# Kernel optimization log

Measured on AMD Instinct MI355X. Metric: run time of the kernel, lower is better.

Reference implementation:

```python
import jax, jax.numpy as jnp
import numpy as np

B, T, J, D = 64, 800, 50, 200  # batch, context len, query len, 2*hidden

def setup_inputs() -> dict:
    key = jax.random.key(0)
    ks = jax.random.split(key, 8)
    return {
        'h':    jax.random.normal(ks[0], (B, T, D), jnp.float32),
        'u':    jax.random.normal(ks[1], (B, J, D), jnp.float32),
        'w_h':  jax.random.normal(ks[2], (D,), jnp.float32) * 0.05,
        'b_h':  jax.random.normal(ks[3], (1,), jnp.float32) * 0.05,
        'w_u':  jax.random.normal(ks[4], (D,), jnp.float32) * 0.05,
        'b_u':  jax.random.normal(ks[5], (1,), jnp.float32) * 0.05,
        'w_hu': jax.random.normal(ks[6], (D,), jnp.float32) * 0.05,
        'b_hu': jax.random.normal(ks[7], (1,), jnp.float32) * 0.05,
    }

def reference(h, u, w_h, b_h, w_u, b_u, w_hu, b_hu):
    # Similarity: s[b,t,j] = ws_h(h_t) + ws_u(u_j) + ws_hu(h_t * u_j)  (+ summed biases)
    # Computed without materializing the [B,T,J,D] expanded tensors of the original.
    sh = jnp.einsum('btd,d->bt', h, w_h)            # [B,T]
    su = jnp.einsum('bjd,d->bj', u, w_u)            # [B,J]
    shu = jnp.einsum('btd,bjd->btj', h * w_hu, u)   # [B,T,J]
    s = shu + sh[:, :, None] + su[:, None, :] + (b_h + b_u + b_hu)[0]
    # Context-to-query attention
    a = jax.nn.softmax(s, axis=2)                   # [B,T,J]
    c2q = jnp.einsum('btj,bjd->btd', a, u)          # [B,T,D]
    # Query-to-context attention
    b = jax.nn.softmax(jnp.max(s, axis=2), axis=1)  # [B,T]
    q2c = jnp.einsum('bt,btd->bd', b, h)[:, None, :]  # [B,1,D], broadcasts over T
    g = jnp.concatenate([h, c2q, h * c2q, h * q2c], axis=-1)  # [B,T,4D]
    return g
```

## Files before the change

kernel.cpp:

```cpp
#include <hip/hip_runtime.h>
#include <cstdint>
#include <cstddef>

#define B_ 64
#define T_ 800
#define J_ 50
#define D_ 200
#define TILE_T 100
#define NTILE 8
#define TT 5
#define NW 4

__device__ __forceinline__ float dot4(float4 a, float4 b) {
    return fmaf(a.x, b.x, fmaf(a.y, b.y, fmaf(a.z, b.z, a.w * b.w)));
}

__global__ __launch_bounds__(256) void k1_kernel(
    const float* __restrict__ h, const float* __restrict__ u,
    const float* __restrict__ w_h, const float* __restrict__ b_h,
    const float* __restrict__ w_u, const float* __restrict__ b_u,
    const float* __restrict__ w_hu, const float* __restrict__ b_hu,
    float* __restrict__ g, float* __restrict__ smax_ws)
{
    __shared__ __align__(16) float4 u4_s[52][51];
    __shared__ __align__(16) float4 whu4_s[50];
    __shared__ __align__(16) float4 wh4_s[50];
    __shared__ __align__(16) float4 wu4_s[50];
    __shared__ float su_s[52];
    __shared__ __align__(16) float4 hw4_s[NW][TT][50];
    __shared__ __align__(16) float a_s[NW][TT][52];

    const int tid  = threadIdx.x;
    const int b    = blockIdx.x / NTILE;
    const int tile = blockIdx.x % NTILE;

    for (int idx = tid; idx < 52 * 50; idx += 256) {
        int j = idx / 50, k = idx - (idx / 50) * 50;
        float4 v = make_float4(0.f, 0.f, 0.f, 0.f);
        if (j < J_) v = *reinterpret_cast<const float4*>(&u[(b * J_ + j) * D_ + 4 * k]);
        u4_s[j][k] = v;
    }
    if (tid < 50) {
        whu4_s[tid] = *reinterpret_cast<const float4*>(&w_hu[4 * tid]);
        wh4_s[tid]  = *reinterpret_cast<const float4*>(&w_h[4 * tid]);
        wu4_s[tid]  = *reinterpret_cast<const float4*>(&w_u[4 * tid]);
    }
    __syncthreads();

    if (tid < 52) {
        float s = b_h[0] + b_u[0] + b_hu[0];
        if (tid < J_) {
            for (int k = 0; k < 50; ++k) s += dot4(u4_s[tid][k], wu4_s[k]);
        }
        su_s[tid] = s;
    }
    __syncthreads();

    const int w    = tid >> 6;
    const int lane = tid & 63;

    float4 whu_r = make_float4(0.f, 0.f, 0.f, 0.f);
    float4 wh_r  = make_float4(0.f, 0.f, 0.f, 0.f);
    if (lane < 50) { whu_r = whu4_s[lane]; wh_r = wh4_s[lane]; }

    const int tbase = tile * TILE_T + w * (TILE_T / NW);
    const int urow  = (lane < 50) ? lane : 50;

    for (int p = 0; p < (TILE_T / NW) / TT; ++p) {
        const int t0 = tbase + p * TT;

        float4 h4r[TT];
        float  shr[TT];
        #pragma unroll
        for (int tt = 0; tt < TT; ++tt) {
            const int t = t0 + tt;
            float4 h4 = make_float4(0.f, 0.f, 0.f, 0.f);
            if (lane < 50)
                h4 = *reinterpret_cast<const float4*>(&h[(size_t)(b * T_ + t) * D_ + 4 * lane]);
            h4r[tt] = h4;
            float4 hw;
            hw.x = h4.x * whu_r.x; hw.y = h4.y * whu_r.y;
            hw.z = h4.z * whu_r.z; hw.w = h4.w * whu_r.w;
            if (lane < 50) hw4_s[w][tt][lane] = hw;
            float ps = dot4(h4, wh_r);
            #pragma unroll
            for (int off = 32; off > 0; off >>= 1) ps += __shfl_xor(ps, off);
            shr[tt] = ps;
        }

        float s[TT];
        {
            const float su = (lane < 50) ? su_s[lane] : 0.f;
            #pragma unroll
            for (int tt = 0; tt < TT; ++tt) s[tt] = su + shr[tt];
        }
        #pragma unroll 2
        for (int k = 0; k < 50; ++k) {
            const float4 u4 = u4_s[urow][k];
            #pragma unroll
            for (int tt = 0; tt < TT; ++tt) {
                const float4 hw = hw4_s[w][tt][k];
                s[tt] += dot4(hw, u4);
            }
        }

        #pragma unroll
        for (int tt = 0; tt < TT; ++tt) {
            float m = (lane < J_) ? s[tt] : -3.4e38f;
            #pragma unroll
            for (int off = 32; off > 0; off >>= 1) m = fmaxf(m, __shfl_xor(m, off));
            float e = (lane < J_) ? __expf(s[tt] - m) : 0.f;
            float sum = e;
            #pragma unroll
            for (int off = 32; off > 0; off >>= 1) sum += __shfl_xor(sum, off);
            const float a = e / sum;
            if (lane < 52) a_s[w][tt][lane] = (lane < J_) ? a : 0.f;
            if (lane == 0) smax_ws[b * T_ + (t0 + tt)] = m;
        }

        float4 c2q[TT];
        #pragma unroll
        for (int tt = 0; tt < TT; ++tt) c2q[tt] = make_float4(0.f, 0.f, 0.f, 0.f);
        const int dcol = (lane < 50) ? lane : 0;
        #pragma unroll 1
        for (int j4 = 0; j4 < 13; ++j4) {
            const float4 ua0 = u4_s[4 * j4 + 0][dcol];
            const float4 ua1 = u4_s[4 * j4 + 1][dcol];
            const float4 ua2 = u4_s[4 * j4 + 2][dcol];
            const float4 ua3 = u4_s[4 * j4 + 3][dcol];
            #pragma unroll
            for (int tt = 0; tt < TT; ++tt) {
                const float4 a4 = *reinterpret_cast<const float4*>(&a_s[w][tt][4 * j4]);
                c2q[tt].x = fmaf(a4.x, ua0.x, c2q[tt].x);
                c2q[tt].y = fmaf(a4.x, ua0.y, c2q[tt].y);
                c2q[tt].z = fmaf(a4.x, ua0.z, c2q[tt].z);
                c2q[tt].w = fmaf(a4.x, ua0.w, c2q[tt].w);
                c2q[tt].x = fmaf(a4.y, ua1.x, c2q[tt].x);
                c2q[tt].y = fmaf(a4.y, ua1.y, c2q[tt].y);
                c2q[tt].z = fmaf(a4.y, ua1.z, c2q[tt].z);
                c2q[tt].w = fmaf(a4.y, ua1.w, c2q[tt].w);
                c2q[tt].x = fmaf(a4.z, ua2.x, c2q[tt].x);
                c2q[tt].y = fmaf(a4.z, ua2.y, c2q[tt].y);
                c2q[tt].z = fmaf(a4.z, ua2.z, c2q[tt].z);
                c2q[tt].w = fmaf(a4.z, ua2.w, c2q[tt].w);
                c2q[tt].x = fmaf(a4.w, ua3.x, c2q[tt].x);
                c2q[tt].y = fmaf(a4.w, ua3.y, c2q[tt].y);
                c2q[tt].z = fmaf(a4.w, ua3.z, c2q[tt].z);
                c2q[tt].w = fmaf(a4.w, ua3.w, c2q[tt].w);
            }
        }

        #pragma unroll
        for (int tt = 0; tt < TT; ++tt) {
            const int t = t0 + tt;
            if (lane < 50) {
                const size_t go = (size_t)(b * T_ + t) * (4 * D_) + 4 * lane;
                *reinterpret_cast<float4*>(&g[go]) = h4r[tt];
                *reinterpret_cast<float4*>(&g[go + D_]) = c2q[tt];
                float4 hc;
                hc.x = h4r[tt].x * c2q[tt].x; hc.y = h4r[tt].y * c2q[tt].y;
                hc.z = h4r[tt].z * c2q[tt].z; hc.w = h4r[tt].w * c2q[tt].w;
                *reinterpret_cast<float4*>(&g[go + 2 * D_]) = hc;
            }
        }
    }
}

__global__ __launch_bounds__(256) void k2_kernel(const float* __restrict__ smax,
                                                 float* __restrict__ bsm,
                                                 float* __restrict__ q2c)
{
    const int b = blockIdx.x, tid = threadIdx.x;
    const int lane = tid & 63, w = tid >> 6;
    __shared__ float redm[4], reds[4];

    float v[4];
    float m = -3.4e38f;
    #pragma unroll
    for (int k = 0; k < 4; ++k) {
        const int t = tid + 256 * k;
        v[k] = (t < T_) ? smax[b * T_ + t] : -3.4e38f;
        m = fmaxf(m, v[k]);
    }
    #pragma unroll
    for (int off = 32; off > 0; off >>= 1) m = fmaxf(m, __shfl_xor(m, off));
    if (lane == 0) redm[w] = m;
    __syncthreads();
    m = fmaxf(fmaxf(redm[0], redm[1]), fmaxf(redm[2], redm[3]));

    float sum = 0.f;
    #pragma unroll
    for (int k = 0; k < 4; ++k) {
        const int t = tid + 256 * k;
        v[k] = (t < T_) ? __expf(v[k] - m) : 0.f;
        sum += v[k];
    }
    #pragma unroll
    for (int off = 32; off > 0; off >>= 1) sum += __shfl_xor(sum, off);
    if (lane == 0) reds[w] = sum;
    __syncthreads();
    sum = reds[0] + reds[1] + reds[2] + reds[3];
    const float inv = 1.f / sum;
    #pragma unroll
    for (int k = 0; k < 4; ++k) {
        const int t = tid + 256 * k;
        if (t < T_) bsm[b * T_ + t] = v[k] * inv;
    }
    if (tid < D_) q2c[b * D_ + tid] = 0.f;
}

__global__ __launch_bounds__(256) void k3_kernel(const float* __restrict__ h,
                                                 const float* __restrict__ bsm,
                                                 float* __restrict__ q2c)
{
    const int b = blockIdx.x / NTILE, tile = blockIdx.x % NTILE;
    const int tid = threadIdx.x;
    __shared__ float bs[TILE_T];
    if (tid < TILE_T) bs[tid] = bsm[b * T_ + tile * TILE_T + tid];
    __syncthreads();
    if (tid < D_) {
        const float* hp = h + ((size_t)b * T_ + tile * TILE_T) * D_ + tid;
        float acc = 0.f;
        #pragma unroll 4
        for (int i = 0; i < TILE_T; ++i) acc = fmaf(bs[i], hp[(size_t)i * D_], acc);
        atomicAdd(&q2c[b * D_ + tid], acc);
    }
}

__global__ __launch_bounds__(256) void k4_kernel(const float* __restrict__ h,
                                                 const float* __restrict__ q2c,
                                                 float* __restrict__ g)
{
    const int b = blockIdx.x / NTILE, tile = blockIdx.x % NTILE;
    const int tid = threadIdx.x;
    __shared__ __align__(16) float4 q4[50];
    if (tid < 50) q4[tid] = *reinterpret_cast<const float4*>(&q2c[b * D_ + 4 * tid]);
    __syncthreads();
    for (int idx = tid; idx < TILE_T * 50; idx += 256) {
        const int tl = idx / 50, l = idx - tl * 50;
        const int t = tile * TILE_T + tl;
        const float4 h4 = *reinterpret_cast<const float4*>(&h[(size_t)(b * T_ + t) * D_ + 4 * l]);
        const float4 q = q4[l];
        float4 o;
        o.x = h4.x * q.x; o.y = h4.y * q.y; o.z = h4.z * q.z; o.w = h4.w * q.w;
        *reinterpret_cast<float4*>(&g[(size_t)(b * T_ + t) * (4 * D_) + 3 * D_ + 4 * l]) = o;
    }
}

extern "C" void kernel_launch(void* const* d_in, const int* in_sizes, int n_in,
                              void* d_out, int out_size, void* d_ws, size_t ws_size,
                              hipStream_t stream)
{
    const float* h    = (const float*)d_in[0];
    const float* u    = (const float*)d_in[1];
    const float* w_h  = (const float*)d_in[2];
    const float* b_h  = (const float*)d_in[3];
    const float* w_u  = (const float*)d_in[4];
    const float* b_u  = (const float*)d_in[5];
    const float* w_hu = (const float*)d_in[6];
    const float* b_hu = (const float*)d_in[7];
    float* g = (float*)d_out;

    float* smax = (float*)d_ws;
    float* bsm  = smax + B_ * T_;
    float* q2c  = bsm + B_ * T_;

    k1_kernel<<<dim3(B_ * NTILE), dim3(256), 0, stream>>>(h, u, w_h, b_h, w_u, b_u, w_hu, b_hu, g, smax);
    k2_kernel<<<dim3(B_), dim3(256), 0, stream>>>(smax, bsm, q2c);
    k3_kernel<<<dim3(B_ * NTILE), dim3(256), 0, stream>>>(h, bsm, q2c);
    k4_kernel<<<dim3(B_ * NTILE), dim3(256), 0, stream>>>(h, q2c, g);
}
```

Measured before the change: 280.1 us.

## Restructure attention kernels: prescaled u tile, readlane c2q, fused softmax into q2c

The main kernel now caches u·w_hu in a rotated shared tile and reads h rows straight from global memory instead of staging h·w_hu in LDS. It computes su per lane from global, and forms c2q by broadcasting each softmax weight with readlane while streaming u rows from global, which drops the a_s LDS buffer. The grid is split into 16 tiles of 50 rows per batch with occupancy hint 4, and q2c zeroing moves into k1. The separate column-softmax kernel is folded into the q2c reduction kernel, which recomputes max and sum per block, leaving three launches instead of four. The trade is more scalar and global loads of h and u, which rely on cache hits, plus redundant softmax reductions across the 8 blocks of each batch.

```diff
diff --git a/kernel.cpp b/kernel.cpp
--- a/kernel.cpp
+++ b/kernel.cpp
@@ -6,82 +6,80 @@
 #define T_ 800
 #define J_ 50
 #define D_ 200
-#define TILE_T 100
-#define NTILE 8
+#define TILE1 50
+#define NTILE1 16
 #define TT 5
-#define NW 4
+#define NPASS 10
 
 __device__ __forceinline__ float dot4(float4 a, float4 b) {
     return fmaf(a.x, b.x, fmaf(a.y, b.y, fmaf(a.z, b.z, a.w * b.w)));
 }
-
-__global__ __launch_bounds__(256) void k1_kernel(
+__device__ __forceinline__ float rlane(float v, int l) {
+    return __int_as_float(__builtin_amdgcn_readlane(__float_as_int(v), l));
+}
+
+__global__ __launch_bounds__(256, 4) void k1_kernel(
     const float* __restrict__ h, const float* __restrict__ u,
     const float* __restrict__ w_h, const float* __restrict__ b_h,
     const float* __restrict__ w_u, const float* __restrict__ b_u,
     const float* __restrict__ w_hu, const float* __restrict__ b_hu,
-    float* __restrict__ g, float* __restrict__ smax_ws)
-{
-    __shared__ __align__(16) float4 u4_s[52][51];
-    __shared__ __align__(16) float4 whu4_s[50];
-    __shared__ __align__(16) float4 wh4_s[50];
-    __shared__ __align__(16) float4 wu4_s[50];
-    __shared__ float su_s[52];
-    __shared__ __align__(16) float4 hw4_s[NW][TT][50];
-    __shared__ __align__(16) float a_s[NW][TT][52];
+    float* __restrict__ g, float* __restrict__ smax_ws, float* __restrict__ q2c)
+{
+    __shared__ __align__(16) float4 uh_s[50][50];
 
     const int tid  = threadIdx.x;
-    const int b    = blockIdx.x / NTILE;
-    const int tile = blockIdx.x % NTILE;
-
-    for (int idx = tid; idx < 52 * 50; idx += 256) {
-        int j = idx / 50, k = idx - (idx / 50) * 50;
-        float4 v = make_float4(0.f, 0.f, 0.f, 0.f);
-        if (j < J_) v = *reinterpret_cast<const float4*>(&u[(b * J_ + j) * D_ + 4 * k]);
-        u4_s[j][k] = v;
-    }
-    if (tid < 50) {
-        whu4_s[tid] = *reinterpret_cast<const float4*>(&w_hu[4 * tid]);
-        wh4_s[tid]  = *reinterpret_cast<const float4*>(&w_h[4 * tid]);
-        wu4_s[tid]  = *reinterpret_cast<const float4*>(&w_u[4 * tid]);
-    }
-    __syncthreads();
-
-    if (tid < 52) {
-        float s = b_h[0] + b_u[0] + b_hu[0];
-        if (tid < J_) {
-            for (int k = 0; k < 50; ++k) s += dot4(u4_s[tid][k], wu4_s[k]);
-        }
-        su_s[tid] = s;
-    }
-    __syncthreads();
-
-    const int w    = tid >> 6;
+    const int b    = blockIdx.x >> 4;
+    const int tile = blockIdx.x & 15;
+
+    if (tile == 0 && tid < D_) q2c[b * D_ + tid] = 0.f;
+
+    for (int idx = tid; idx < 2500; idx += 256) {
+        const int j = idx / 50, k = idx - (idx / 50) * 50;
+        const float4 uu = *reinterpret_cast<const float4*>(&u[(b * J_ + j) * D_ + 4 * k]);
+        const float4 ww = *reinterpret_cast<const float4*>(&w_hu[4 * k]);
+        float4 p; p.x = uu.x * ww.x; p.y = uu.y * ww.y; p.z = uu.z * ww.z; p.w = uu.w * ww.w;
+        int kk = k + ((j >> 2) & 7); if (kk >= 50) kk -= 50;
+        uh_s[j][kk] = p;
+    }
+
     const int lane = tid & 63;
-
-    float4 whu_r = make_float4(0.f, 0.f, 0.f, 0.f);
-    float4 wh_r  = make_float4(0.f, 0.f, 0.f, 0.f);
-    if (lane < 50) { whu_r = whu4_s[lane]; wh_r = wh4_s[lane]; }
-
-    const int tbase = tile * TILE_T + w * (TILE_T / NW);
-    const int urow  = (lane < 50) ? lane : 50;
-
-    for (int p = 0; p < (TILE_T / NW) / TT; ++p) {
-        const int t0 = tbase + p * TT;
+    const int wfl  = __builtin_amdgcn_readfirstlane(tid >> 6);
+
+    float4 wh_r = make_float4(0.f, 0.f, 0.f, 0.f);
+    if (lane < 50) wh_r = *reinterpret_cast<const float4*>(&w_h[4 * lane]);
+
+    float su = b_h[0] + b_u[0] + b_hu[0];
+    {
+        const int j = (lane < J_) ? lane : 0;
+        const float* ur = u + (size_t)(b * J_ + j) * D_;
+        #pragma unroll 5
+        for (int k = 0; k < 50; ++k) {
+            const float4 uu = *reinterpret_cast<const float4*>(&ur[4 * k]);
+            su = fmaf(uu.x, w_u[4 * k + 0], su);
+            su = fmaf(uu.y, w_u[4 * k + 1], su);
+            su = fmaf(uu.z, w_u[4 * k + 2], su);
+            su = fmaf(uu.w, w_u[4 * k + 3], su);
+        }
+    }
+    __syncthreads();
+
+    const int urow = (lane < 50) ? lane : 49;
+    const int crot = (urow >> 2) & 7;
+    const int dcol = (lane < 50) ? lane : 0;
+
+    for (int p = wfl; p < NPASS; p += 4) {
+        const int t0 = tile * TILE1 + p * TT;
 
         float4 h4r[TT];
         float  shr[TT];
+        const float* hrow[TT];
         #pragma unroll
         for (int tt = 0; tt < TT; ++tt) {
             const int t = t0 + tt;
+            hrow[tt] = h + (size_t)(b * T_ + t) * D_;
             float4 h4 = make_float4(0.f, 0.f, 0.f, 0.f);
-            if (lane < 50)
-                h4 = *reinterpret_cast<const float4*>(&h[(size_t)(b * T_ + t) * D_ + 4 * lane]);
+            if (lane < 50) h4 = *reinterpret_cast<const float4*>(&hrow[tt][4 * lane]);
             h4r[tt] = h4;
-            float4 hw;
-            hw.x = h4.x * whu_r.x; hw.y = h4.y * whu_r.y;
-            hw.z = h4.z * whu_r.z; hw.w = h4.w * whu_r.w;
-            if (lane < 50) hw4_s[w][tt][lane] = hw;
             float ps = dot4(h4, wh_r);
             #pragma unroll
             for (int off = 32; off > 0; off >>= 1) ps += __shfl_xor(ps, off);
@@ -89,21 +87,25 @@
         }
 
         float s[TT];
-        {
-            const float su = (lane < 50) ? su_s[lane] : 0.f;
-            #pragma unroll
-            for (int tt = 0; tt < TT; ++tt) s[tt] = su + shr[tt];
-        }
-        #pragma unroll 2
+        #pragma unroll
+        for (int tt = 0; tt < TT; ++tt) s[tt] = su + shr[tt];
+        #pragma unroll 5
         for (int k = 0; k < 50; ++k) {
-            const float4 u4 = u4_s[urow][k];
+            int kk = k + crot; if (kk >= 50) kk -= 50;
+            const float4 uh = uh_s[urow][kk];
             #pragma unroll
             for (int tt = 0; tt < TT; ++tt) {
-                const float4 hw = hw4_s[w][tt][k];
-                s[tt] += dot4(hw, u4);
+                const float* hr = hrow[tt];
+                float acc = s[tt];
+                acc = fmaf(uh.x, hr[4 * k + 0], acc);
+                acc = fmaf(uh.y, hr[4 * k + 1], acc);
+                acc = fmaf(uh.z, hr[4 * k + 2], acc);
+                acc = fmaf(uh.w, hr[4 * k + 3], acc);
+                s[tt] = acc;
             }
         }
 
+        float a[TT];
         #pragma unroll
         for (int tt = 0; tt < TT; ++tt) {
             float m = (lane < J_) ? s[tt] : -3.4e38f;
@@ -113,40 +115,24 @@
             float sum = e;
             #pragma unroll
             for (int off = 32; off > 0; off >>= 1) sum += __shfl_xor(sum, off);
-            const float a = e / sum;
-            if (lane < 52) a_s[w][tt][lane] = (lane < J_) ? a : 0.f;
+            a[tt] = e / sum;
             if (lane == 0) smax_ws[b * T_ + (t0 + tt)] = m;
         }
 
         float4 c2q[TT];
         #pragma unroll
         for (int tt = 0; tt < TT; ++tt) c2q[tt] = make_float4(0.f, 0.f, 0.f, 0.f);
-        const int dcol = (lane < 50) ? lane : 0;
-        #pragma unroll 1
-        for (int j4 = 0; j4 < 13; ++j4) {
-            const float4 ua0 = u4_s[4 * j4 + 0][dcol];
-            const float4 ua1 = u4_s[4 * j4 + 1][dcol];
-            const float4 ua2 = u4_s[4 * j4 + 2][dcol];
-            const float4 ua3 = u4_s[4 * j4 + 3][dcol];
+        const float* ub = u + (size_t)b * J_ * D_;
+        #pragma unroll 2
+        for (int j = 0; j < J_; ++j) {
+            const float4 uc = *reinterpret_cast<const float4*>(&ub[(size_t)j * D_ + 4 * dcol]);
             #pragma unroll
             for (int tt = 0; tt < TT; ++tt) {
-                const float4 a4 = *reinterpret_cast<const float4*>(&a_s[w][tt][4 * j4]);
-                c2q[tt].x = fmaf(a4.x, ua0.x, c2q[tt].x);
-                c2q[tt].y = fmaf(a4.x, ua0.y, c2q[tt].y);
-                c2q[tt].z = fmaf(a4.x, ua0.z, c2q[tt].z);
-                c2q[tt].w = fmaf(a4.x, ua0.w, c2q[tt].w);
-                c2q[tt].x = fmaf(a4.y, ua1.x, c2q[tt].x);
-                c2q[tt].y = fmaf(a4.y, ua1.y, c2q[tt].y);
-                c2q[tt].z = fmaf(a4.y, ua1.z, c2q[tt].z);
-                c2q[tt].w = fmaf(a4.y, ua1.w, c2q[tt].w);
-                c2q[tt].x = fmaf(a4.z, ua2.x, c2q[tt].x);
-                c2q[tt].y = fmaf(a4.z, ua2.y, c2q[tt].y);
-                c2q[tt].z = fmaf(a4.z, ua2.z, c2q[tt].z);
-                c2q[tt].w = fmaf(a4.z, ua2.w, c2q[tt].w);
-                c2q[tt].x = fmaf(a4.w, ua3.x, c2q[tt].x);
-                c2q[tt].y = fmaf(a4.w, ua3.y, c2q[tt].y);
-                c2q[tt].z = fmaf(a4.w, ua3.z, c2q[tt].z);
-                c2q[tt].w = fmaf(a4.w, ua3.w, c2q[tt].w);
+                const float ab = rlane(a[tt], j);
+                c2q[tt].x = fmaf(ab, uc.x, c2q[tt].x);
+                c2q[tt].y = fmaf(ab, uc.y, c2q[tt].y);
+                c2q[tt].z = fmaf(ab, uc.z, c2q[tt].z);
+                c2q[tt].w = fmaf(ab, uc.w, c2q[tt].w);
             }
         }
 
@@ -166,13 +152,15 @@
     }
 }
 
-__global__ __launch_bounds__(256) void k2_kernel(const float* __restrict__ smax,
-                                                 float* __restrict__ bsm,
+__global__ __launch_bounds__(256) void k3_kernel(const float* __restrict__ h,
+                                                 const float* __restrict__ smax,
                                                  float* __restrict__ q2c)
 {
-    const int b = blockIdx.x, tid = threadIdx.x;
-    const int lane = tid & 63, w = tid >> 6;
-    __shared__ float redm[4], reds[4];
+    const int b = blockIdx.x >> 3, t8 = blockIdx.x & 7;
+    const int rows0 = t8 * 100;
+    const int tid = threadIdx.x, lane = tid & 63, w = tid >> 6;
+    __shared__ float red[4];
+    __shared__ float bs[100];
 
     float v[4];
     float m = -3.4e38f;
@@ -184,45 +172,32 @@
     }
     #pragma unroll
     for (int off = 32; off > 0; off >>= 1) m = fmaxf(m, __shfl_xor(m, off));
-    if (lane == 0) redm[w] = m;
-    __syncthreads();
-    m = fmaxf(fmaxf(redm[0], redm[1]), fmaxf(redm[2], redm[3]));
+    if (lane == 0) red[w] = m;
+    __syncthreads();
+    m = fmaxf(fmaxf(red[0], red[1]), fmaxf(red[2], red[3]));
+    __syncthreads();
 
     float sum = 0.f;
     #pragma unroll
     for (int k = 0; k < 4; ++k) {
         const int t = tid + 256 * k;
-        v[k] = (t < T_) ? __expf(v[k] - m) : 0.f;
-        sum += v[k];
+        sum += (t < T_) ? __expf(v[k] - m) : 0.f;
     }
     #pragma unroll
     for (int off = 32; off > 0; off >>= 1) sum += __shfl_xor(sum, off);
-    if (lane == 0) reds[w] = sum;
-    __syncthreads();
-    sum = reds[0] + reds[1] + reds[2] + reds[3];
+    if (lane == 0) red[w] = sum;
+    __syncthreads();
+    sum = red[0] + red[1] + red[2] + red[3];
     const float inv = 1.f / sum;
-    #pragma unroll
-    for (int k = 0; k < 4; ++k) {
-        const int t = tid + 256 * k;
-        if (t < T_) bsm[b * T_ + t] = v[k] * inv;
-    }
-    if (tid < D_) q2c[b * D_ + tid] = 0.f;
-}
-
-__global__ __launch_bounds__(256) void k3_kernel(const float* __restrict__ h,
-                                                 const float* __restrict__ bsm,
-                                                 float* __restrict__ q2c)
-{
-    const int b = blockIdx.x / NTILE, tile = blockIdx.x % NTILE;
-    const int tid = threadIdx.x;
-    __shared__ float bs[TILE_T];
-    if (tid < TILE_T) bs[tid] = bsm[b * T_ + tile * TILE_T + tid];
-    __syncthreads();
+
+    if (tid < 100) bs[tid] = __expf(smax[b * T_ + rows0 + tid] - m) * inv;
+    __syncthreads();
+
     if (tid < D_) {
-        const float* hp = h + ((size_t)b * T_ + tile * TILE_T) * D_ + tid;
+        const float* hp = h + ((size_t)b * T_ + rows0) * D_ + tid;
         float acc = 0.f;
-        #pragma unroll 4
-        for (int i = 0; i < TILE_T; ++i) acc = fmaf(bs[i], hp[(size_t)i * D_], acc);
+        #pragma unroll 10
+        for (int i = 0; i < 100; ++i) acc = fmaf(bs[i], hp[(size_t)i * D_], acc);
         atomicAdd(&q2c[b * D_ + tid], acc);
     }
 }
@@ -231,19 +206,19 @@
                                                  const float* __restrict__ q2c,
                                                  float* __restrict__ g)
 {
-    const int b = blockIdx.x / NTILE, tile = blockIdx.x % NTILE;
+    const int b = blockIdx.x >> 4, tc = blockIdx.x & 15;
     const int tid = threadIdx.x;
-    __shared__ __align__(16) float4 q4[50];
-    if (tid < 50) q4[tid] = *reinterpret_cast<const float4*>(&q2c[b * D_ + 4 * tid]);
-    __syncthreads();
-    for (int idx = tid; idx < TILE_T * 50; idx += 256) {
-        const int tl = idx / 50, l = idx - tl * 50;
-        const int t = tile * TILE_T + tl;
-        const float4 h4 = *reinterpret_cast<const float4*>(&h[(size_t)(b * T_ + t) * D_ + 4 * l]);
-        const float4 q = q4[l];
+    if (tid >= 250) return;
+    const int tl = tid / 50, d4 = tid - tl * 50;
+    const float4 q = *reinterpret_cast<const float4*>(&q2c[b * D_ + 4 * d4]);
+    const int trow0 = tc * 50 + tl;
+    #pragma unroll 5
+    for (int i = 0; i < 10; ++i) {
+        const int t = trow0 + 5 * i;
+        const float4 h4 = *reinterpret_cast<const float4*>(&h[(size_t)(b * T_ + t) * D_ + 4 * d4]);
         float4 o;
         o.x = h4.x * q.x; o.y = h4.y * q.y; o.z = h4.z * q.z; o.w = h4.w * q.w;
-        *reinterpret_cast<float4*>(&g[(size_t)(b * T_ + t) * (4 * D_) + 3 * D_ + 4 * l]) = o;
+        *reinterpret_cast<float4*>(&g[(size_t)(b * T_ + t) * (4 * D_) + 3 * D_ + 4 * d4]) = o;
     }
 }
 
@@ -262,11 +237,9 @@
     float* g = (float*)d_out;
 
     float* smax = (float*)d_ws;
-    float* bsm  = smax + B_ * T_;
-    float* q2c  = bsm + B_ * T_;
-
-    k1_kernel<<<dim3(B_ * NTILE), dim3(256), 0, stream>>>(h, u, w_h, b_h, w_u, b_u, w_hu, b_hu, g, smax);
-    k2_kernel<<<dim3(B_), dim3(256), 0, stream>>>(smax, bsm, q2c);
-    k3_kernel<<<dim3(B_ * NTILE), dim3(256), 0, stream>>>(h, bsm, q2c);
-    k4_kernel<<<dim3(B_ * NTILE), dim3(256), 0, stream>>>(h, q2c, g);
-}
+    float* q2c  = smax + B_ * T_;
+
+    k1_kernel<<<dim3(B_ * NTILE1), dim3(256), 0, stream>>>(h, u, w_h, b_h, w_u, b_u, w_hu, b_hu, g, smax, q2c);
+    k3_kernel<<<dim3(B_ * 8), dim3(256), 0, stream>>>(h, smax, q2c);
+    k4_kernel<<<dim3(B_ * NTILE1), dim3(256), 0, stream>>>(h, q2c, g);
+}
```

New measurement: 304.3 us. 8.7% more time.
